# Optimization experiments

Hardware: AMD Instinct MI355X
Metric: run time of the kernel (lower is better)

Reference implementation:

```python
import jax, jax.numpy as jnp
import numpy as np

B, C, H, W = 4, 256, 128, 128
HEADS = 64
HD = C // HEADS  # 4
G = 32           # group norm groups
EPS = 1e-5


def setup_inputs() -> dict:
    key = jax.random.key(0)
    ks = jax.random.split(key, 6)
    x = jax.random.normal(ks[0], (B, C, H, W), dtype=jnp.float32)
    gn_weight = jnp.ones((1, C, 1, 1), dtype=jnp.float32)
    gn_bias = jnp.zeros((1, C, 1, 1), dtype=jnp.float32)
    # 1x1 convs stored as (out_ch, in_ch) matrices
    qkv_w = jax.random.normal(ks[1], (3 * C, C), dtype=jnp.float32) * 0.02
    qkv_b = jax.random.normal(ks[2], (3 * C,), dtype=jnp.float32) * 0.01
    out_w = jax.random.normal(ks[3], (C, C), dtype=jnp.float32) * 0.02
    out_b = jax.random.normal(ks[4], (C,), dtype=jnp.float32) * 0.01
    return {"x": x, "gn_weight": gn_weight, "gn_bias": gn_bias,
            "qkv_w": qkv_w, "qkv_b": qkv_b, "out_w": out_w, "out_b": out_b}


def group_norm(x, weight, bias):
    n, c, h, w = x.shape
    xg = x.reshape(n, G, -1)
    mean = xg.mean(axis=-1, keepdims=True)
    var = jnp.var(xg, axis=-1, keepdims=True, ddof=1)  # torch.var default is unbiased
    xg = (xg - mean) / jnp.sqrt(var + EPS)
    return xg.reshape(n, c, h, w) * weight + bias


def conv1x1(x, w, b):
    # x: (B, Cin, H, W), w: (Cout, Cin)
    return jnp.einsum('bchw,oc->bohw', x, w) + b[None, :, None, None]


def reference(x, gn_weight, gn_bias, qkv_w, qkv_b, out_w, out_b):
    skip = x
    h = group_norm(x, gn_weight, gn_bias)
    qkv = conv1x1(h, qkv_w, qkv_b)                      # (B, 3C, H, W)
    qkv = qkv.reshape(B, HEADS, 3 * HD, H * W)
    q, k, v = jnp.split(qkv, 3, axis=2)                  # each (B, heads, hd, HW)
    scores = jnp.einsum('bhdn,bhen->bhde', q, k) / (HD ** 0.5)  # (B, heads, hd, hd)
    scores = jax.nn.softmax(scores, axis=1)              # softmax over HEADS axis (as in source)
    out = jnp.einsum('bhde,bhen->bhdn', scores, v)       # (B, heads, hd, HW)
    out = out.reshape(B, C, H, W)
    out = conv1x1(out, out_w, out_b)
    return out + skip
```

## Files before the change

kernel.cpp:

```cpp
#include <hip/hip_runtime.h>


constexpr int kB = 4;
constexpr int kC = 256;
constexpr int kHW = 16384;
constexpr int kHeads = 64;
constexpr int kNG = 32;
constexpr int kCPG = 8;
constexpr int kCP1 = 257;
constexpr int kPS = 260;
constexpr float kEPS = 1e-5f;
constexpr int kNSplit = 32;

typedef __attribute__((ext_vector_type(8))) _Float16 f16x8;
typedef __attribute__((ext_vector_type(4))) _Float16 f16x4;
typedef __attribute__((ext_vector_type(4))) float f32x4;

union V8 { f16x8 v; uint4 u; _Float16 h[8]; };

__device__ __forceinline__ void gload16(const void* g, void* l) {
  __builtin_amdgcn_global_load_lds(
      (const __attribute__((address_space(1))) void*)g,
      (__attribute__((address_space(3))) void*)l, 16, 0, 0);
}

constexpr size_t oXH    = 0;
constexpr size_t oSpart = oXH + (size_t)kB * kHW * kC / 2;
constexpr size_t oS     = oSpart + (size_t)3 * kB * kNSplit * 128 * 128;
constexpr size_t oSums  = oS + (size_t)kB * kCP1 * kPS;
constexpr size_t oGv    = oSums + (size_t)kB * kC;
constexpr size_t oScore = oGv + (size_t)kB * kC;
constexpr size_t oM     = oScore + (size_t)kB * kHeads * 16;
constexpr size_t oGmH   = oM + (size_t)kB * kC * kPS;

__global__ __launch_bounds__(256) void k0_cast(const float* __restrict__ x,
                                               _Float16* __restrict__ xH,
                                               float* __restrict__ sums) {
  const int seg = blockIdx.x, c = blockIdx.y, b = blockIdx.z;
  const int tid = threadIdx.x;
  const size_t base = ((size_t)b * kC + c) * kHW + (size_t)seg * 4096 + tid * 16;
  float4 v0 = *(const float4*)(x + base);
  float4 v1 = *(const float4*)(x + base + 4);
  float4 v2 = *(const float4*)(x + base + 8);
  float4 v3 = *(const float4*)(x + base + 12);
  V8 h0, h1;
  h0.h[0] = (_Float16)v0.x; h0.h[1] = (_Float16)v0.y;
  h0.h[2] = (_Float16)v0.z; h0.h[3] = (_Float16)v0.w;
  h0.h[4] = (_Float16)v1.x; h0.h[5] = (_Float16)v1.y;
  h0.h[6] = (_Float16)v1.z; h0.h[7] = (_Float16)v1.w;
  h1.h[0] = (_Float16)v2.x; h1.h[1] = (_Float16)v2.y;
  h1.h[2] = (_Float16)v2.z; h1.h[3] = (_Float16)v2.w;
  h1.h[4] = (_Float16)v3.x; h1.h[5] = (_Float16)v3.y;
  h1.h[6] = (_Float16)v3.z; h1.h[7] = (_Float16)v3.w;
  *(uint4*)(xH + base) = h0.u;
  *(uint4*)(xH + base + 8) = h1.u;
  float rs = (v0.x + v0.y + v0.z + v0.w) + (v1.x + v1.y + v1.z + v1.w) +
             (v2.x + v2.y + v2.z + v2.w) + (v3.x + v3.y + v3.z + v3.w);
#pragma unroll
  for (int off = 32; off; off >>= 1) rs += __shfl_xor(rs, off);
  __shared__ float ps[4];
  if ((tid & 63) == 0) ps[tid >> 6] = rs;
  __syncthreads();
  if (tid == 0) atomicAdd(&sums[b * kC + c], ps[0] + ps[1] + ps[2] + ps[3]);
}

__global__ __launch_bounds__(256) void k1_syrk(const _Float16* __restrict__ xH,
                                               float* __restrict__ Spart) {
  const int tt = blockIdx.x >> 5;
  const int sp = blockIdx.x & 31;
  const int b = blockIdx.y;
  const int ti = (tt == 2) ? 1 : 0;
  const int tj = (tt == 0) ? 0 : 1;
  const bool diag = (ti == tj);
  const _Float16* xb = xH + (size_t)b * kC * kHW;
  const int n0 = sp * (kHW / kNSplit);

  __shared__ __align__(16) _Float16 XI[2][128 * 64];
  __shared__ __align__(16) _Float16 XJ[2][128 * 64];

  const int tid = threadIdx.x;
  const int wave = tid >> 6, lane = tid & 63;
  const int wi = wave >> 1, wj = wave & 1;
  const int lrow = lane & 15, lgq = lane >> 4;
  const int srow = lane >> 3, sslot = lane & 7;

  const _Float16* srcI = xb + (size_t)(ti * 128) * kHW + n0;
  const _Float16* srcJ = xb + (size_t)(tj * 128) * kHW + n0;

  f32x4 acc[16];
#pragma unroll
  for (int i = 0; i < 16; ++i) acc[i] = (f32x4){0.f, 0.f, 0.f, 0.f};

  auto stage = [&](int buf, int nb) {
#pragma unroll
    for (int rep = 0; rep < 4; ++rep) {
      const int rr = rep * 32 + wave * 8 + srow;
      const int g = sslot ^ (rr & 7);
      char* dI = (char*)XI[buf] + (rep * 32 + wave * 8) * 128;
      gload16(srcI + (size_t)rr * kHW + nb + g * 8, dI);
      if (!diag) {
        char* dJ = (char*)XJ[buf] + (rep * 32 + wave * 8) * 128;
        gload16(srcJ + (size_t)rr * kHW + nb + g * 8, dJ);
      }
    }
  };

  stage(0, 0);
  __syncthreads();

  constexpr int NCH = kHW / kNSplit / 64;
  for (int ch = 0; ch < NCH; ++ch) {
    const int buf = ch & 1;
    if (ch + 1 < NCH) stage(buf ^ 1, (ch + 1) * 64);
    const _Float16* XIb = XI[buf];
    const _Float16* XBb = diag ? XI[buf] : XJ[buf];
#pragma unroll
    for (int sub = 0; sub < 2; ++sub) {
      const int gq = sub * 4 + lgq;
      f16x8 afr[4], bfr[4];
#pragma unroll
      for (int ia = 0; ia < 4; ++ia) {
        const int r = wi * 64 + ia * 16 + lrow;
        afr[ia] = *(const f16x8*)((const char*)XIb + (size_t)r * 128 + (((unsigned)(gq ^ (r & 7))) << 4));
      }
#pragma unroll
      for (int jb = 0; jb < 4; ++jb) {
        const int r = wj * 64 + jb * 16 + lrow;
        bfr[jb] = *(const f16x8*)((const char*)XBb + (size_t)r * 128 + (((unsigned)(gq ^ (r & 7))) << 4));
      }
#pragma unroll
      for (int ia = 0; ia < 4; ++ia)
#pragma unroll
        for (int jb = 0; jb < 4; ++jb)
          acc[ia * 4 + jb] = __builtin_amdgcn_mfma_f32_16x16x32_f16(afr[ia], bfr[jb], acc[ia * 4 + jb], 0, 0, 0);
    }
    __syncthreads();
  }
  float* P = Spart + (((size_t)tt * kB + b) * kNSplit + sp) * 16384;
#pragma unroll
  for (int ia = 0; ia < 4; ++ia)
#pragma unroll
    for (int jb = 0; jb < 4; ++jb)
#pragma unroll
      for (int reg = 0; reg < 4; ++reg) {
        const int i = wi * 64 + ia * 16 + lgq * 4 + reg;
        const int j = wj * 64 + jb * 16 + lrow;
        P[(size_t)i * 128 + j] = acc[ia * 4 + jb][reg];
      }
}

__global__ __launch_bounds__(256) void k1r_reduce(const float* __restrict__ Spart,
                                                  float* __restrict__ S) {
  const int blk = blockIdx.x;
  const int tile12 = blk >> 5;
  const int part = blk & 31;
  const int tt = tile12 >> 2, b = tile12 & 3;
  const int rti = (tt == 2) ? 1 : 0;
  const int rtj = (tt == 0) ? 0 : 1;
  const int e0 = part * 512 + threadIdx.x * 2;
  float2 s = {0.f, 0.f};
  const float* base = Spart + ((size_t)tt * kB + b) * kNSplit * 16384 + e0;
#pragma unroll 8
  for (int sp = 0; sp < kNSplit; ++sp) {
    float2 v = *(const float2*)(base + (size_t)sp * 16384);
    s.x += v.x; s.y += v.y;
  }
  const int i = e0 >> 7, j = e0 & 127;
  float* Sb = S + (size_t)b * kCP1 * kPS;
  float* dst = Sb + (size_t)(rti * 128 + i) * kPS + rtj * 128 + j;
  dst[0] = s.x; dst[1] = s.y;
  if (tt == 1) {
    Sb[(size_t)(128 + j + 0) * kPS + i] = s.x;
    Sb[(size_t)(128 + j + 1) * kPS + i] = s.y;
  }
}

__global__ __launch_bounds__(256) void k3ab(const float* __restrict__ S,
                                            const float* __restrict__ sums,
                                            const float* __restrict__ gw,
                                            const float* __restrict__ gb,
                                            const float* __restrict__ qkv_w,
                                            const float* __restrict__ qkv_b,
                                            float* __restrict__ score) {
  const int h = blockIdx.x, b = blockIdx.y;
  const float* Sb = S + (size_t)b * kCP1 * kPS;
  const float HWf = (float)kHW;
  __shared__ float shx[kC], shd[kC];
  __shared__ float meanv[kNG], invv[kNG];
  __shared__ float4 suw[kC];
  __shared__ float redPQ[4][8];
  __shared__ float red16[4][16];
  const int tid = threadIdx.x;
  const int wave = tid >> 6, lane = tid & 63;

  shx[tid] = sums[b * kC + tid];
  shd[tid] = Sb[(size_t)tid * kPS + tid];
  __syncthreads();
  if (tid < kNG) {
    float sum = 0.f, ssq = 0.f;
#pragma unroll
    for (int k = 0; k < kCPG; ++k) { sum += shx[tid * kCPG + k]; ssq += shd[tid * kCPG + k]; }
    const float n = (float)(kCPG * kHW);
    const float mean = sum / n;
    const float var = (ssq - n * mean * mean) / (n - 1.0f);
    meanv[tid] = mean;
    invv[tid] = rsqrtf(var + kEPS);
  }
  __syncthreads();
  const float s_c = gw[tid] * invv[tid / kCPG];
  const float t_c = gb[tid] - meanv[tid / kCPG] * s_c;
  const float x_c = shx[tid];
  const float r_c = s_c * x_c + t_c * HWf;

  const float u0 = qkv_w[(size_t)(h * 12 + 0) * kC + tid];
  const float u1 = qkv_w[(size_t)(h * 12 + 1) * kC + tid];
  const float u2 = qkv_w[(size_t)(h * 12 + 2) * kC + tid];
  const float u3 = qkv_w[(size_t)(h * 12 + 3) * kC + tid];
  const float v0 = qkv_w[(size_t)(h * 12 + 4) * kC + tid];
  const float v1 = qkv_w[(size_t)(h * 12 + 5) * kC + tid];
  const float v2 = qkv_w[(size_t)(h * 12 + 6) * kC + tid];
  const float v3 = qkv_w[(size_t)(h * 12 + 7) * kC + tid];
  suw[tid] = make_float4(u0 * s_c, u1 * s_c, u2 * s_c, u3 * s_c);

  float p[8] = {u0 * s_c * x_c, u1 * s_c * x_c, u2 * s_c * x_c, u3 * s_c * x_c,
                u0 * t_c, u1 * t_c, u2 * t_c, u3 * t_c};
#pragma unroll
  for (int i = 0; i < 8; ++i)
#pragma unroll
    for (int off = 32; off; off >>= 1) p[i] += __shfl_xor(p[i], off);
  if (lane == 0) {
#pragma unroll
    for (int i = 0; i < 8; ++i) redPQ[wave][i] = p[i];
  }
  __syncthreads();
  float P[4], Qp[4];
#pragma unroll
  for (int d = 0; d < 4; ++d) {
    P[d]  = redPQ[0][d] + redPQ[1][d] + redPQ[2][d] + redPQ[3][d];
    Qp[d] = redPQ[0][4 + d] + redPQ[1][4 + d] + redPQ[2][4 + d] + redPQ[3][4 + d]
            + qkv_b[h * 12 + d];
  }

  float sd0 = 0.f, sd1 = 0.f, sd2 = 0.f, sd3 = 0.f;
#pragma unroll 8
  for (int c = 0; c < kC; ++c) {
    const float Sval = Sb[(size_t)c * kPS + tid];
    const float4 w = suw[c];
    sd0 += w.x * Sval; sd1 += w.y * Sval; sd2 += w.z * Sval; sd3 += w.w * Sval;
  }
  float wd[4];
#pragma unroll
  for (int d = 0; d < 4; ++d) {
    const float sdv = (d == 0) ? sd0 : (d == 1) ? sd1 : (d == 2) ? sd2 : sd3;
    wd[d] = s_c * sdv + t_c * P[d] + r_c * Qp[d];
  }
  const float sv[4] = {v0, v1, v2, v3};
  float pr[16];
#pragma unroll
  for (int d = 0; d < 4; ++d)
#pragma unroll
    for (int e = 0; e < 4; ++e) pr[d * 4 + e] = wd[d] * sv[e];
#pragma unroll
  for (int i = 0; i < 16; ++i)
#pragma unroll
    for (int off = 32; off; off >>= 1) pr[i] += __shfl_xor(pr[i], off);
  if (lane == 0) {
#pragma unroll
    for (int i = 0; i < 16; ++i) red16[wave][i] = pr[i];
  }
  __syncthreads();
  if (tid < 16) {
    const int d = tid >> 2, e = tid & 3;
    float tot = red16[0][tid] + red16[1][tid] + red16[2][tid] + red16[3][tid];
    const float w256 = P[d] + HWf * Qp[d];
    tot += w256 * qkv_b[h * 12 + 4 + e];
    score[((size_t)(b * kHeads) + h) * 16 + tid] = 0.5f * tot;
  }
}

__global__ __launch_bounds__(256) void k45_M(const float* __restrict__ score,
                                             const float* __restrict__ qkv_w,
                                             const float* __restrict__ qkv_b,
                                             float* __restrict__ M) {
  const int b = blockIdx.y;
  const int cidx = blockIdx.x;
  const int h = cidx >> 2, d = cidx & 3;
  __shared__ float sc[64][4];
  __shared__ float mx[4], sm[4];
  const int tid = threadIdx.x;
  {
    const int h2 = tid >> 2, e = tid & 3;
    sc[h2][e] = score[((size_t)(b * kHeads) + h2) * 16 + d * 4 + e];
  }
  __syncthreads();
  const int wave = tid >> 6, lane = tid & 63;
  {
    const float v = sc[lane][wave];
    float m = v;
#pragma unroll
    for (int off = 32; off; off >>= 1) m = fmaxf(m, __shfl_xor(m, off));
    float e2 = expf(v - m);
#pragma unroll
    for (int off = 32; off; off >>= 1) e2 += __shfl_xor(e2, off);
    if (lane == 0) { mx[wave] = m; sm[wave] = e2; }
  }
  __syncthreads();
  const float p0 = expf(sc[h][0] - mx[0]) / sm[0];
  const float p1 = expf(sc[h][1] - mx[1]) / sm[1];
  const float p2 = expf(sc[h][2] - mx[2]) / sm[2];
  const float p3 = expf(sc[h][3] - mx[3]) / sm[3];
  for (int cp = tid; cp < kCP1; cp += 256) {
    float a;
    if (cp < kC) {
      a = p0 * qkv_w[(size_t)(h * 12 + 8 + 0) * kC + cp] +
          p1 * qkv_w[(size_t)(h * 12 + 8 + 1) * kC + cp] +
          p2 * qkv_w[(size_t)(h * 12 + 8 + 2) * kC + cp] +
          p3 * qkv_w[(size_t)(h * 12 + 8 + 3) * kC + cp];
    } else {
      a = p0 * qkv_b[h * 12 + 8 + 0] + p1 * qkv_b[h * 12 + 8 + 1] +
          p2 * qkv_b[h * 12 + 8 + 2] + p3 * qkv_b[h * 12 + 8 + 3];
    }
    M[((size_t)b * kC + cidx) * kPS + cp] = a;
  }
}

__global__ __launch_bounds__(256) void k5b_gemm(const float* __restrict__ M,
                                                const float* __restrict__ out_w,
                                                const float* __restrict__ S,
                                                const float* __restrict__ sums,
                                                const float* __restrict__ gw,
                                                const float* __restrict__ gb,
                                                _Float16* __restrict__ GmH,
                                                float* __restrict__ gvec) {
  const int ct = blockIdx.x, ot = blockIdx.y, b = blockIdx.z;
  const float* Mb = M + (size_t)b * kC * kPS;
  const float* Sb = S + (size_t)b * kCP1 * kPS;
  __shared__ float Wt[32][68];
  __shared__ float Gs[32][68];
  __shared__ float gred[64][17];
  __shared__ float sS[kC], sT[kC];
  __shared__ float meanv[kNG], invv[kNG];
  const int tid = threadIdx.x;
  sS[tid] = sums[b * kC + tid];
  sT[tid] = Sb[(size_t)tid * kPS + tid];
  __syncthreads();
  if (tid < kNG) {
    float sum = 0.f, ssq = 0.f;
#pragma unroll
    for (int k = 0; k < kCPG; ++k) { sum += sS[tid * kCPG + k]; ssq += sT[tid * kCPG + k]; }
    const float n = (float)(kCPG * kHW);
    const float mean = sum / n;
    const float var = (ssq - n * mean * mean) / (n - 1.0f);
    meanv[tid] = mean;
    invv[tid] = rsqrtf(var + kEPS);
  }
  __syncthreads();
  {
    const float sv = gw[tid] * invv[tid / kCPG];
    sS[tid] = sv;
    sT[tid] = gb[tid] - meanv[tid / kCPG] * sv;
  }
  __syncthreads();
  float acc[16];
#pragma unroll
  for (int i = 0; i < 16; ++i) acc[i] = 0.f;
  const int i0 = (tid & 15) * 4;
  const int j0 = (tid >> 4) * 4;
  const int cp0 = ct * 64;

  for (int cb = 0; cb < kC; cb += 32) {
    int idx = tid;
#pragma unroll
    for (int r = 0; r < 2; ++r) {
      const int m = idx >> 3;
      const int c4 = (idx & 7) * 4;
      float4 v = *(const float4*)(out_w + (size_t)(ot * 64 + m) * kC + cb + c4);
      Wt[c4 + 0][m] = v.x; Wt[c4 + 1][m] = v.y; Wt[c4 + 2][m] = v.z; Wt[c4 + 3][m] = v.w;
      idx += 256;
    }
    idx = tid;
#pragma unroll
    for (int r = 0; r < 2; ++r) {
      const int cc = idx >> 4;
      const int n4 = (idx & 15) * 4;
      float4 v = {0.f, 0.f, 0.f, 0.f};
      if (cp0 + n4 < kCP1) v = *(const float4*)(Mb + (size_t)(cb + cc) * kPS + cp0 + n4);
      *(float4*)&Gs[cc][n4] = v;
      idx += 256;
    }
    __syncthreads();
#pragma unroll
    for (int kk = 0; kk < 32; ++kk) {
      float4 a = *(const float4*)&Wt[kk][i0];
      float4 g = *(const float4*)&Gs[kk][j0];
      acc[0]  += a.x * g.x; acc[1]  += a.x * g.y; acc[2]  += a.x * g.z; acc[3]  += a.x * g.w;
      acc[4]  += a.y * g.x; acc[5]  += a.y * g.y; acc[6]  += a.y * g.z; acc[7]  += a.y * g.w;
      acc[8]  += a.z * g.x; acc[9]  += a.z * g.y; acc[10] += a.z * g.z; acc[11] += a.z * g.w;
      acc[12] += a.w * g.x; acc[13] += a.w * g.y; acc[14] += a.w * g.z; acc[15] += a.w * g.w;
    }
    __syncthreads();
  }
  float gpart[4] = {0.f, 0.f, 0.f, 0.f};
#pragma unroll
  for (int mi = 0; mi < 4; ++mi) {
    const int o = ot * 64 + i0 + mi;
#pragma unroll
    for (int cj = 0; cj < 4; ++cj) {
      const int cp = cp0 + j0 + cj;
      const float f = acc[mi * 4 + cj];
      if (cp < kC) {
        GmH[((size_t)b * kC + o) * kC + cp] = (_Float16)(f * sS[cp]);
        gpart[mi] += f * sT[cp];
      } else if (cp == kC) {
        gpart[mi] += f;
      }
    }
  }
#pragma unroll
  for (int mi = 0; mi < 4; ++mi) gred[i0 + mi][tid >> 4] = gpart[mi];
  __syncthreads();
  if (tid < 64) {
    float s = 0.f;
#pragma unroll
    for (int k = 0; k < 16; ++k) s += gred[tid][k];
    atomicAdd(&gvec[b * kC + ot * 64 + tid], s);
  }
}

__global__ __launch_bounds__(256) void k6_final(const _Float16* __restrict__ xH,
                                                const _Float16* __restrict__ GmH,
                                                const float* __restrict__ gvec,
                                                const float* __restrict__ out_b,
                                                const float* __restrict__ x,
                                                float* __restrict__ out) {
  const int nt = blockIdx.x, ot = blockIdx.y, b = blockIdx.z;
  __shared__ __align__(16) char smem[64 * 132 * 4];
  _Float16* GT = (_Float16*)smem;
  _Float16* XT = (_Float16*)(smem + 16384);
  float* Ep = (float*)smem;
  const int tid = threadIdx.x;
  const int wave = tid >> 6, lane = tid & 63;
  const int wo = wave >> 1, wn = wave & 1;
  const int lrow = lane & 15, lgq = lane >> 4;
  const int xc = tid >> 2, xq = tid & 3;

  f32x4 acc[16];
#pragma unroll
  for (int i = 0; i < 16; ++i) acc[i] = (f32x4){0.f, 0.f, 0.f, 0.f};

  for (int cc = 0; cc < kC; cc += 64) {
#pragma unroll
    for (int rep = 0; rep < 4; ++rep) {
      const int gi = tid + rep * 256;
      const int r = gi >> 3, g = gi & 7;
      const size_t boff = (size_t)r * 128 + (((unsigned)(g ^ ((r ^ (r >> 3)) & 7))) << 4);
      uint4 gv = *(const uint4*)(GmH + ((size_t)(b * kC + ot * 128 + r)) * kC + cc + g * 8);
      *(uint4*)((char*)GT + boff) = gv;
    }
    {
      const _Float16* xrow = xH + ((size_t)b * kC + cc + xc) * kHW + nt * 128;
#pragma unroll
      for (int rep = 0; rep < 4; ++rep) {
        const int n0 = rep * 32 + xq * 8;
        V8 hx; hx.u = *(const uint4*)(xrow + n0);
#pragma unroll
        for (int k = 0; k < 8; ++k) {
          const int n = n0 + k;
          *(_Float16*)((char*)XT + (size_t)n * 128 +
                       (((unsigned)((xc >> 3) ^ ((n ^ (n >> 3)) & 7))) << 4) +
                       (xc & 7) * 2) = hx.h[k];
        }
      }
    }
    __syncthreads();
#pragma unroll
    for (int sub = 0; sub < 2; ++sub) {
      const int gq = sub * 4 + lgq;
      f16x8 afr[4], bfr[4];
#pragma unroll
      for (int ia = 0; ia < 4; ++ia) {
        const int r = wo * 64 + ia * 16 + lrow;
        afr[ia] = *(const f16x8*)((const char*)GT + (size_t)r * 128 +
                                  (((unsigned)(gq ^ ((r ^ (r >> 3)) & 7))) << 4));
      }
#pragma unroll
      for (int jb = 0; jb < 4; ++jb) {
        const int r = wn * 64 + jb * 16 + lrow;
        bfr[jb] = *(const f16x8*)((const char*)XT + (size_t)r * 128 +
                                  (((unsigned)(gq ^ ((r ^ (r >> 3)) & 7))) << 4));
      }
#pragma unroll
      for (int ia = 0; ia < 4; ++ia)
#pragma unroll
        for (int jb = 0; jb < 4; ++jb)
          acc[ia * 4 + jb] = __builtin_amdgcn_mfma_f32_16x16x32_f16(afr[ia], bfr[jb], acc[ia * 4 + jb], 0, 0, 0);
    }
    __syncthreads();
  }
#pragma unroll
  for (int p = 0; p < 2; ++p) {
    if (wo == p) {
#pragma unroll
      for (int ia = 0; ia < 4; ++ia)
#pragma unroll
        for (int jb = 0; jb < 4; ++jb)
#pragma unroll
          for (int reg = 0; reg < 4; ++reg)
            Ep[(size_t)(ia * 16 + lgq * 4 + reg) * 132 + wn * 64 + jb * 16 + lrow] =
                acc[ia * 4 + jb][reg];
    }
    __syncthreads();
#pragma unroll
    for (int it = 0; it < 8; ++it) {
      const int id = it * 256 + tid;
      const int row = id >> 5, nc = (id & 31) * 4;
      const int o = ot * 128 + p * 64 + row;
      const float gvv = gvec[b * kC + o] + out_b[o];
      float4 e = *(const float4*)&Ep[(size_t)row * 132 + nc];
      const size_t gidx = ((size_t)b * kC + o) * kHW + nt * 128 + nc;
      float4 sk = *(const float4*)&x[gidx];
      float4 res = {e.x + gvv + sk.x, e.y + gvv + sk.y, e.z + gvv + sk.z, e.w + gvv + sk.w};
      *(float4*)&out[gidx] = res;
    }
    __syncthreads();
  }
}

extern "C" void kernel_launch(void* const* d_in, const int* in_sizes, int n_in,
                              void* d_out, int out_size, void* d_ws, size_t ws_size,
                              hipStream_t stream) {
  const float* x    = (const float*)d_in[0];
  const float* gnw  = (const float*)d_in[1];
  const float* gnb  = (const float*)d_in[2];
  const float* qkvw = (const float*)d_in[3];
  const float* qkvb = (const float*)d_in[4];
  const float* outw = (const float*)d_in[5];
  const float* outb = (const float*)d_in[6];
  float* out = (float*)d_out;
  float* ws = (float*)d_ws;

  _Float16* xH   = (_Float16*)(ws + oXH);
  float* Spart   = ws + oSpart;
  float* S       = ws + oS;
  float* sums    = ws + oSums;
  float* gv      = ws + oGv;
  float* score   = ws + oScore;
  float* M       = ws + oM;
  _Float16* GmH  = (_Float16*)(ws + oGmH);

  hipMemsetAsync(sums, 0, (size_t)2 * kB * kC * sizeof(float), stream);
  k0_cast<<<dim3(4, kC, kB), 256, 0, stream>>>(x, xH, sums);
  k1_syrk<<<dim3(3 * kNSplit, kB), 256, 0, stream>>>(xH, Spart);
  k1r_reduce<<<dim3(3 * kB * 32), 256, 0, stream>>>(Spart, S);
  k3ab<<<dim3(kHeads, kB), 256, 0, stream>>>(S, sums, gnw, gnb, qkvw, qkvb, score);
  k45_M<<<dim3(kC, kB), 256, 0, stream>>>(score, qkvw, qkvb, M);
  k5b_gemm<<<dim3(5, 4, kB), 256, 0, stream>>>(M, outw, S, sums, gnw, gnb, GmH, gv);
  k6_final<<<dim3(kHW / 128, kC / 128, kB), 256, 0, stream>>>(xH, GmH, gv, outb, x, out);
}
```

Measured before the change: 208.5 us.

## Fuse softmax/M construction into output GEMM and reorder syrk block mapping

Removes the separate k45_M kernel. k5b_gemm now computes the head-axis softmax probabilities itself and builds the M tile on the fly from qkv_w/qkv_b while staging Gs, which drops one launch and the M workspace round trip. Separately, k1_syrk remaps blockIdx so that blocks of all three tile types sharing the same spatial split run together, to improve L2 reuse of xH. The cost is that every GEMM block recomputes the softmax, and the staging loop now does more global reads and arithmetic.

```diff
diff --git a/kernel.cpp b/kernel.cpp
--- a/kernel.cpp
+++ b/kernel.cpp
@@ -30,8 +30,7 @@
 constexpr size_t oSums  = oS + (size_t)kB * kCP1 * kPS;
 constexpr size_t oGv    = oSums + (size_t)kB * kC;
 constexpr size_t oScore = oGv + (size_t)kB * kC;
-constexpr size_t oM     = oScore + (size_t)kB * kHeads * 16;
-constexpr size_t oGmH   = oM + (size_t)kB * kC * kPS;
+constexpr size_t oGmH   = oScore + (size_t)kB * kHeads * 16;
 
 __global__ __launch_bounds__(256) void k0_cast(const float* __restrict__ x,
                                                _Float16* __restrict__ xH,
@@ -66,8 +65,10 @@
 
 __global__ __launch_bounds__(256) void k1_syrk(const _Float16* __restrict__ xH,
                                                float* __restrict__ Spart) {
-  const int tt = blockIdx.x >> 5;
-  const int sp = blockIdx.x & 31;
+  const int bx = blockIdx.x;
+  const int chunk = bx / 24, rr0 = bx % 24;
+  const int tt = rr0 >> 3;
+  const int sp = chunk * 8 + (rr0 & 7);
   const int b = blockIdx.y;
   const int ti = (tt == 2) ? 1 : 0;
   const int tj = (tt == 0) ? 0 : 1;
@@ -278,71 +279,33 @@
   }
 }
 
-__global__ __launch_bounds__(256) void k45_M(const float* __restrict__ score,
-                                             const float* __restrict__ qkv_w,
-                                             const float* __restrict__ qkv_b,
-                                             float* __restrict__ M) {
-  const int b = blockIdx.y;
-  const int cidx = blockIdx.x;
-  const int h = cidx >> 2, d = cidx & 3;
-  __shared__ float sc[64][4];
-  __shared__ float mx[4], sm[4];
-  const int tid = threadIdx.x;
-  {
-    const int h2 = tid >> 2, e = tid & 3;
-    sc[h2][e] = score[((size_t)(b * kHeads) + h2) * 16 + d * 4 + e];
-  }
-  __syncthreads();
-  const int wave = tid >> 6, lane = tid & 63;
-  {
-    const float v = sc[lane][wave];
-    float m = v;
-#pragma unroll
-    for (int off = 32; off; off >>= 1) m = fmaxf(m, __shfl_xor(m, off));
-    float e2 = expf(v - m);
-#pragma unroll
-    for (int off = 32; off; off >>= 1) e2 += __shfl_xor(e2, off);
-    if (lane == 0) { mx[wave] = m; sm[wave] = e2; }
-  }
-  __syncthreads();
-  const float p0 = expf(sc[h][0] - mx[0]) / sm[0];
-  const float p1 = expf(sc[h][1] - mx[1]) / sm[1];
-  const float p2 = expf(sc[h][2] - mx[2]) / sm[2];
-  const float p3 = expf(sc[h][3] - mx[3]) / sm[3];
-  for (int cp = tid; cp < kCP1; cp += 256) {
-    float a;
-    if (cp < kC) {
-      a = p0 * qkv_w[(size_t)(h * 12 + 8 + 0) * kC + cp] +
-          p1 * qkv_w[(size_t)(h * 12 + 8 + 1) * kC + cp] +
-          p2 * qkv_w[(size_t)(h * 12 + 8 + 2) * kC + cp] +
-          p3 * qkv_w[(size_t)(h * 12 + 8 + 3) * kC + cp];
-    } else {
-      a = p0 * qkv_b[h * 12 + 8 + 0] + p1 * qkv_b[h * 12 + 8 + 1] +
-          p2 * qkv_b[h * 12 + 8 + 2] + p3 * qkv_b[h * 12 + 8 + 3];
-    }
-    M[((size_t)b * kC + cidx) * kPS + cp] = a;
-  }
-}
-
-__global__ __launch_bounds__(256) void k5b_gemm(const float* __restrict__ M,
-                                                const float* __restrict__ out_w,
+__global__ __launch_bounds__(256) void k5b_gemm(const float* __restrict__ out_w,
                                                 const float* __restrict__ S,
                                                 const float* __restrict__ sums,
                                                 const float* __restrict__ gw,
                                                 const float* __restrict__ gb,
+                                                const float* __restrict__ score,
+                                                const float* __restrict__ qkv_w,
+                                                const float* __restrict__ qkv_b,
                                                 _Float16* __restrict__ GmH,
                                                 float* __restrict__ gvec) {
   const int ct = blockIdx.x, ot = blockIdx.y, b = blockIdx.z;
-  const float* Mb = M + (size_t)b * kC * kPS;
   const float* Sb = S + (size_t)b * kCP1 * kPS;
   __shared__ float Wt[32][68];
   __shared__ float Gs[32][68];
   __shared__ float gred[64][17];
   __shared__ float sS[kC], sT[kC];
   __shared__ float meanv[kNG], invv[kNG];
+  __shared__ float scs[kHeads * 16];
+  __shared__ float pw[kC][4];
+  __shared__ float mxp[16], smp[16];
+  __shared__ float wred[4][16];
   const int tid = threadIdx.x;
+  const int wave = tid >> 6, lane = tid & 63;
+
   sS[tid] = sums[b * kC + tid];
   sT[tid] = Sb[(size_t)tid * kPS + tid];
+  *(float4*)&scs[tid * 4] = ((const float4*)(score + (size_t)b * kHeads * 16))[tid];
   __syncthreads();
   if (tid < kNG) {
     float sum = 0.f, ssq = 0.f;
@@ -354,13 +317,42 @@
     meanv[tid] = mean;
     invv[tid] = rsqrtf(var + kEPS);
   }
-  __syncthreads();
   {
+    const int p = tid & 15, hh = tid >> 4;
+    float m = scs[(hh * 4 + 0) * 16 + p];
+#pragma unroll
+    for (int k = 1; k < 4; ++k) m = fmaxf(m, scs[(hh * 4 + k) * 16 + p]);
+    m = fmaxf(m, __shfl_xor(m, 16));
+    m = fmaxf(m, __shfl_xor(m, 32));
+    if (lane < 16) wred[wave][lane] = m;
+  }
+  __syncthreads();
+  if (tid < 16) mxp[tid] = fmaxf(fmaxf(wred[0][tid], wred[1][tid]),
+                                 fmaxf(wred[2][tid], wred[3][tid]));
+  __syncthreads();
+  {
+    const int p = tid & 15, hh = tid >> 4;
+    float s = 0.f;
+#pragma unroll
+    for (int k = 0; k < 4; ++k) s += expf(scs[(hh * 4 + k) * 16 + p] - mxp[p]);
+    s += __shfl_xor(s, 16);
+    s += __shfl_xor(s, 32);
+    if (lane < 16) wred[wave][lane] = s;
+  }
+  __syncthreads();
+  if (tid < 16) smp[tid] = wred[0][tid] + wred[1][tid] + wred[2][tid] + wred[3][tid];
+  __syncthreads();
+  {
+    const int h = tid >> 2, d = tid & 3;
+#pragma unroll
+    for (int e = 0; e < 4; ++e)
+      pw[tid][e] = expf(scs[h * 16 + d * 4 + e] - mxp[d * 4 + e]) / smp[d * 4 + e];
     const float sv = gw[tid] * invv[tid / kCPG];
     sS[tid] = sv;
     sT[tid] = gb[tid] - meanv[tid / kCPG] * sv;
   }
   __syncthreads();
+
   float acc[16];
 #pragma unroll
   for (int i = 0; i < 16; ++i) acc[i] = 0.f;
@@ -383,9 +375,29 @@
     for (int r = 0; r < 2; ++r) {
       const int cc = idx >> 4;
       const int n4 = (idx & 15) * 4;
-      float4 v = {0.f, 0.f, 0.f, 0.f};
-      if (cp0 + n4 < kCP1) v = *(const float4*)(Mb + (size_t)(cb + cc) * kPS + cp0 + n4);
-      *(float4*)&Gs[cc][n4] = v;
+      const int cidx = cb + cc;
+      const int h = cidx >> 2;
+      const float4 pv = *(const float4*)&pw[cidx][0];
+      const int cp = cp0 + n4;
+      float4 o;
+      if (cp < kC) {
+        const float* w0 = qkv_w + (size_t)(h * 12 + 8) * kC + cp;
+        const float4 a0 = *(const float4*)(w0);
+        const float4 a1 = *(const float4*)(w0 + kC);
+        const float4 a2 = *(const float4*)(w0 + 2 * kC);
+        const float4 a3 = *(const float4*)(w0 + 3 * kC);
+        o.x = pv.x * a0.x + pv.y * a1.x + pv.z * a2.x + pv.w * a3.x;
+        o.y = pv.x * a0.y + pv.y * a1.y + pv.z * a2.y + pv.w * a3.y;
+        o.z = pv.x * a0.z + pv.y * a1.z + pv.z * a2.z + pv.w * a3.z;
+        o.w = pv.x * a0.w + pv.y * a1.w + pv.z * a2.w + pv.w * a3.w;
+      } else if (cp == kC) {
+        const float bs = pv.x * qkv_b[h * 12 + 8] + pv.y * qkv_b[h * 12 + 9] +
+                         pv.z * qkv_b[h * 12 + 10] + pv.w * qkv_b[h * 12 + 11];
+        o = (float4){bs, 0.f, 0.f, 0.f};
+      } else {
+        o = (float4){0.f, 0.f, 0.f, 0.f};
+      }
+      *(float4*)&Gs[cc][n4] = o;
       idx += 256;
     }
     __syncthreads();
@@ -545,7 +557,6 @@
   float* sums    = ws + oSums;
   float* gv      = ws + oGv;
   float* score   = ws + oScore;
-  float* M       = ws + oM;
   _Float16* GmH  = (_Float16*)(ws + oGmH);
 
   hipMemsetAsync(sums, 0, (size_t)2 * kB * kC * sizeof(float), stream);
@@ -553,7 +564,7 @@
   k1_syrk<<<dim3(3 * kNSplit, kB), 256, 0, stream>>>(xH, Spart);
   k1r_reduce<<<dim3(3 * kB * 32), 256, 0, stream>>>(Spart, S);
   k3ab<<<dim3(kHeads, kB), 256, 0, stream>>>(S, sums, gnw, gnb, qkvw, qkvb, score);
-  k45_M<<<dim3(kC, kB), 256, 0, stream>>>(score, qkvw, qkvb, M);
-  k5b_gemm<<<dim3(5, 4, kB), 256, 0, stream>>>(M, outw, S, sums, gnw, gnb, GmH, gv);
+  k5b_gemm<<<dim3(5, 4, kB), 256, 0, stream>>>(outw, S, sums, gnw, gnb, score,
+                                               qkvw, qkvb, GmH, gv);
   k6_final<<<dim3(kHW / 128, kC / 128, kB), 256, 0, stream>>>(xH, GmH, gv, outb, x, out);
 }
```

Result: no change. 205.9 us (median of 2 runs) (-1.3%).
